# Optimization experiments

Measured on AMD Instinct MI355X. Metric: run time of the kernel, lower is better.

## Reference

```python
import jax, jax.numpy as jnp
import numpy as np

B, T, D = 256, 512, 8      # batch, seq_len, Feature_number
H = 120                    # hidden_size
L = 4                      # layers=['s','s','s','s']
NH = D                     # num_heads = Feature_number
HD = H // NH               # head dim = 15
EPS = 1e-5


def setup_inputs() -> dict:
    key = jax.random.key(0)
    ks = jax.random.split(key, 16)
    rn = lambda k, shape, s=0.1: (jax.random.normal(k, shape, jnp.float32) * s)
    return {
        "x":   jax.random.normal(ks[0], (B, T, D), jnp.float32),
        # input->gate weights, stacked over layers
        "Wi":  rn(ks[1], (L, H, D)),
        "Wf":  rn(ks[2], (L, H, D)),
        "Wz":  rn(ks[3], (L, H, D)),
        "Wo":  rn(ks[4], (L, H, D)),
        # block-diagonal (multi-head) recurrent weights: [L, NH, HD, HD]
        "Ri":  rn(ks[5], (L, NH, HD, HD)),
        "Rf":  rn(ks[6], (L, NH, HD, HD)),
        "Rz":  rn(ks[7], (L, NH, HD, HD)),
        "Ro":  rn(ks[8], (L, NH, HD, HD)),
        "bi":  rn(ks[9],  (L, H), 0.02),
        "bf":  rn(ks[10], (L, H), 0.02),
        "bz":  rn(ks[11], (L, H), 0.02),
        "bo":  rn(ks[12], (L, H), 0.02),
        # per-block down-projection back to Feature_number (residual block)
        "Wp":  rn(ks[13], (L, D, H)),
        "bp":  jnp.zeros((L, D), jnp.float32),
        # BatchNorm1d(Feature_number) affine params
        "gamma": jnp.ones((D,), jnp.float32),
        "beta":  jnp.zeros((D,), jnp.float32),
        # fc5: Linear(Feature_number, 1)
        "Wfc": rn(ks[14], (1, D)),
        "bfc": jnp.zeros((1,), jnp.float32),
    }


def _slstm_layer(x, Wi, Wf, Wz, Wo, Ri, Rf, Rz, Ro, bi, bf, bz, bo, Wp, bp):
    """One sLSTM block: exp-gated recurrence with stabilizer, then down-proj + residual.
    x: [B, T, D] -> [B, T, D]."""
    Bn = x.shape[0]

    def rec(h, R):  # block-diagonal recurrent matmul: [B,H] x [NH,HD,HD] -> [B,H]
        return jnp.einsum("bnd,nde->bne", h.reshape(Bn, NH, HD), R).reshape(Bn, H)

    def step(carry, x_t):
        h, c, n, m = carry                       # each [B, H]
        it = x_t @ Wi.T + rec(h, Ri) + bi        # input gate pre-act
        ft = x_t @ Wf.T + rec(h, Rf) + bf        # forget gate pre-act (exp gating)
        z = jnp.tanh(x_t @ Wz.T + rec(h, Rz) + bz)
        o = jax.nn.sigmoid(x_t @ Wo.T + rec(h, Ro) + bo)
        m_new = jnp.maximum(ft + m, it)          # stabilizer state
        i_p = jnp.exp(it - m_new)
        f_p = jnp.exp(ft + m - m_new)
        c_new = f_p * c + i_p * z
        n_new = f_p * n + i_p                    # normalizer state
        h_new = o * (c_new / n_new)
        return (h_new, c_new, n_new, m_new), h_new

    z0 = jnp.zeros((Bn, H), x.dtype)
    (_, _, _, _), hs = jax.lax.scan(step, (z0, z0, z0, z0), jnp.swapaxes(x, 0, 1))
    y = jnp.einsum("tbh,dh->tbd", hs, Wp) + bp   # down-project to D
    return x + jnp.swapaxes(y, 0, 1)             # residual


def reference(x, Wi, Wf, Wz, Wo, Ri, Rf, Rz, Ro, bi, bf, bz, bo, Wp, bp,
              gamma, beta, Wfc, bfc):
    h = x
    for l in range(L):
        h = _slstm_layer(h, Wi[l], Wf[l], Wz[l], Wo[l], Ri[l], Rf[l], Rz[l], Ro[l],
                         bi[l], bf[l], bz[l], bo[l], Wp[l], bp[l])
    last = h[:, -1, :]                            # [B, D]
    # BatchNorm1d in training mode (batch stats, biased variance)
    mu = jnp.mean(last, axis=0)
    var = jnp.mean((last - mu) ** 2, axis=0)
    bn = (last - mu) / jnp.sqrt(var + EPS) * gamma + beta
    out = jax.nn.sigmoid(bn @ Wfc.T + bfc)        # [B, 1]
    return out[:, 0]                              # squeeze(1) -> [B]
```

## Files before the change

### kernel.cpp

```cpp
#include <hip/hip_runtime.h>
#include <math.h>

#define Bsz 256
#define T   512
#define Dd  8
#define Hh  120
#define Ll  4
#define NHn 8
#define HDd 15
#define HP  20
#define EPSf 1e-5f

__device__ __forceinline__ float fast_rcp(float x) {
#if __has_builtin(__builtin_amdgcn_rcpf)
    return __builtin_amdgcn_rcpf(x);
#else
    return 1.f / x;
#endif
}
__device__ __forceinline__ float tanh_fast(float x) {
    float e = __expf(2.f * x);
    return 1.f - 2.f * fast_rcp(e + 1.f);
}
__device__ __forceinline__ float sigm_fast(float x) {
    return fast_rcp(1.f + __expf(-x));
}

__global__
__attribute__((amdgpu_flat_work_group_size(512, 512)))
__attribute__((amdgpu_waves_per_eu(2, 2)))
void slstm_kernel(
    const float* __restrict__ x,
    const float* __restrict__ Wi, const float* __restrict__ Wf,
    const float* __restrict__ Wz, const float* __restrict__ Wo,
    const float* __restrict__ Ri, const float* __restrict__ Rf,
    const float* __restrict__ Rz, const float* __restrict__ Ro,
    const float* __restrict__ bi, const float* __restrict__ bf,
    const float* __restrict__ bz, const float* __restrict__ bo,
    const float* __restrict__ Wp, const float* __restrict__ bp,
    float* __restrict__ last_out)
{
    __shared__ __align__(16) float xs[T * Dd];
    __shared__ __align__(16) float hb[Ll][2][NHn * HP];

    const int tid = threadIdx.x;
    const int b   = blockIdx.x;
    const int l   = tid >> 7;
    const int j   = tid & 127;

    {
        const float4* xg  = (const float4*)(x + (size_t)b * T * Dd);
        float4*       xs4 = (float4*)xs;
        xs4[tid]       = xg[tid];
        xs4[tid + 512] = xg[tid + 512];
        float* hbf = (float*)hb;
        hbf[tid]       = 0.f;
        hbf[tid + 512] = 0.f;
        if (tid < 256) hbf[tid + 1024] = 0.f;
    }

    const bool gl = (j < Hh);
    const int jj  = gl ? j : 0;
    const int n   = jj / HDd;
    const int e   = jj - n * HDd;
    float wI[Dd], wF[Dd], wZ[Dd], wO[Dd];
    float rI[HDd], rF[HDd], rZ[HDd], rO[HDd];
    {
        const int row = (l * Hh + jj) * Dd;
#pragma unroll
        for (int d = 0; d < Dd; ++d) {
            wI[d] = Wi[row + d]; wF[d] = Wf[row + d];
            wZ[d] = Wz[row + d]; wO[d] = Wo[row + d];
        }
        const int rb = ((l * NHn + n) * HDd) * HDd + e;
#pragma unroll
        for (int d = 0; d < HDd; ++d) {
            rI[d] = Ri[rb + d * HDd]; rF[d] = Rf[rb + d * HDd];
            rZ[d] = Rz[rb + d * HDd]; rO[d] = Ro[rb + d * HDd];
        }
    }
    float bI = bi[l * Hh + jj], bF = bf[l * Hh + jj];
    float bZ = bz[l * Hh + jj], bO = bo[l * Hh + jj];

    const int p  = (j >= 64) ? (j - 64) : j;
    const int d8 = p & 7, ch = p >> 3;
    float wp_r[16];
    {
        const int base = l * Dd * Hh + d8 * Hh + ch * HDd;
#pragma unroll
        for (int k = 0; k < HDd; ++k) wp_r[k] = Wp[base + k];
        wp_r[15] = 0.f;
    }
    float bp_r = bp[l * Dd + d8];

    float cst = 0.f, nst = 0.f, mst = 0.f;

    __syncthreads();

    for (int tau = 0; tau < T + 2 * Ll - 1; ++tau) {
        const int t_g = tau - 2 * l;
        const int t_p = t_g - 1;

        if (gl && (t_g >= 0) && (t_g < T)) {
            const float4* xt4 = (const float4*)(xs + t_g * Dd);
            const float4 xa = xt4[0], xb2 = xt4[1];
            const float xv[Dd] = {xa.x, xa.y, xa.z, xa.w, xb2.x, xb2.y, xb2.z, xb2.w};
            float gi = bI, gf = bF, gz = bZ, go = bO;
#pragma unroll
            for (int d = 0; d < Dd; ++d) {
                gi = fmaf(xv[d], wI[d], gi);
                gf = fmaf(xv[d], wF[d], gf);
                gz = fmaf(xv[d], wZ[d], gz);
                go = fmaf(xv[d], wO[d], go);
            }
            const float4* h4 = (const float4*)(&hb[l][t_g & 1][n * HP]);
            const float4 h0 = h4[0], h1 = h4[1], h2 = h4[2], h3 = h4[3];
            const float hv[16] = {h0.x, h0.y, h0.z, h0.w, h1.x, h1.y, h1.z, h1.w,
                                  h2.x, h2.y, h2.z, h2.w, h3.x, h3.y, h3.z, h3.w};
#pragma unroll
            for (int d = 0; d < HDd; ++d) {
                gi = fmaf(hv[d], rI[d], gi);
                gf = fmaf(hv[d], rF[d], gf);
                gz = fmaf(hv[d], rZ[d], gz);
                go = fmaf(hv[d], rO[d], go);
            }
            const float z  = tanh_fast(gz);
            const float o  = sigm_fast(go);
            const float mn = fmaxf(gf + mst, gi);
            const float ip = __expf(gi - mn);
            const float fp = __expf(gf + mst - mn);
            cst = fmaf(fp, cst, ip * z);
            nst = fmaf(fp, nst, ip);
            mst = mn;
            hb[l][(t_g & 1) ^ 1][n * HP + e] = o * cst * fast_rcp(nst);
        }

        if ((j >= 64) && (t_p >= 0) && (t_p < T)) {
            const float4* h4 = (const float4*)(&hb[l][t_g & 1][ch * HP]);
            const float4 h0 = h4[0], h1 = h4[1], h2 = h4[2], h3 = h4[3];
            const float hv[16] = {h0.x, h0.y, h0.z, h0.w, h1.x, h1.y, h1.z, h1.w,
                                  h2.x, h2.y, h2.z, h2.w, h3.x, h3.y, h3.z, h3.w};
            float s = 0.f;
#pragma unroll
            for (int k = 0; k < 16; ++k) s = fmaf(hv[k], wp_r[k], s);
            s += __shfl_xor(s, 8);
            s += __shfl_xor(s, 16);
            s += __shfl_xor(s, 32);
            if (p < Dd) xs[t_p * Dd + p] += s + bp_r;
        }

        __syncthreads();
    }

    if (tid < Dd) last_out[b * Dd + tid] = xs[(T - 1) * Dd + tid];
}

__global__ __launch_bounds__(Bsz) void bn_fc_kernel(
    const float* __restrict__ last,
    const float* __restrict__ gamma, const float* __restrict__ beta,
    const float* __restrict__ Wfc,   const float* __restrict__ bfc,
    float* __restrict__ out)
{
    __shared__ __align__(16) float ls[Bsz][Dd];
    __shared__ float rsum[32][Dd], rsq[32][Dd];
    __shared__ float mu[Dd], rstdg[Dd], bet[Dd], wfc[Dd];
    const int tid = threadIdx.x;
    {
        const float4* lg = (const float4*)last;
        ((float4*)ls)[tid]       = lg[tid];
        ((float4*)ls)[tid + 256] = lg[tid + 256];
    }
    __syncthreads();
    {
        const int d = tid & 7, g = tid >> 3;
        float s = 0.f, q = 0.f;
#pragma unroll
        for (int k = 0; k < 8; ++k) {
            const float v = ls[g + 32 * k][d];
            s += v; q = fmaf(v, v, q);
        }
        rsum[g][d] = s; rsq[g][d] = q;
    }
    __syncthreads();
    if (tid < Dd) {
        float s = 0.f, q = 0.f;
#pragma unroll
        for (int g = 0; g < 32; ++g) { s += rsum[g][tid]; q += rsq[g][tid]; }
        const float mean = s * (1.f / Bsz);
        const float var  = q * (1.f / Bsz) - mean * mean;
        mu[tid]    = mean;
        rstdg[tid] = rsqrtf(fmaxf(var, 0.f) + EPSf) * gamma[tid];
        bet[tid]   = beta[tid];
        wfc[tid]   = Wfc[tid];
    }
    __syncthreads();
    float acc = bfc[0];
#pragma unroll
    for (int d = 0; d < Dd; ++d)
        acc += ((ls[tid][d] - mu[d]) * rstdg[d] + bet[d]) * wfc[d];
    out[tid] = sigm_fast(acc);
}

extern "C" void kernel_launch(void* const* d_in, const int* in_sizes, int n_in,
                              void* d_out, int out_size, void* d_ws, size_t ws_size,
                              hipStream_t stream) {
    const float* x    = (const float*)d_in[0];
    const float* Wi   = (const float*)d_in[1];
    const float* Wf   = (const float*)d_in[2];
    const float* Wz   = (const float*)d_in[3];
    const float* Wo   = (const float*)d_in[4];
    const float* Ri   = (const float*)d_in[5];
    const float* Rf   = (const float*)d_in[6];
    const float* Rz   = (const float*)d_in[7];
    const float* Ro   = (const float*)d_in[8];
    const float* bi   = (const float*)d_in[9];
    const float* bf   = (const float*)d_in[10];
    const float* bz   = (const float*)d_in[11];
    const float* bo   = (const float*)d_in[12];
    const float* Wp   = (const float*)d_in[13];
    const float* bp   = (const float*)d_in[14];
    const float* gamma= (const float*)d_in[15];
    const float* beta = (const float*)d_in[16];
    const float* Wfc  = (const float*)d_in[17];
    const float* bfc  = (const float*)d_in[18];

    float* last_ws = (float*)d_ws;
    float* out     = (float*)d_out;

    slstm_kernel<<<Bsz, 512, 0, stream>>>(x, Wi, Wf, Wz, Wo, Ri, Rf, Rz, Ro,
                                          bi, bf, bz, bo, Wp, bp, last_ws);
    bn_fc_kernel<<<1, Bsz, 0, stream>>>(last_ws, gamma, beta, Wfc, bfc, out);
}
```

Before: 466.4 us.

## Pack two hidden units per lane and shrink block to one wave per layer

Each layer now runs in a single 64-lane wave, with every active lane computing two hidden units instead of one. The block shrinks from 512 to 256 threads. The down-projection weights move from registers to shared memory so the same wave can also do the projection. This cuts idle lanes and lets the per-layer work stay inside one wavefront, at the cost of twice the serial math per lane per timestep and more register pressure.

Measured after the change: 616.7 us. +32.2%, slower.

```diff
diff --git a/kernel.cpp b/kernel.cpp
--- a/kernel.cpp
+++ b/kernel.cpp
@@ -26,9 +26,48 @@
     return fast_rcp(1.f + __expf(-x));
 }
 
+#define LD16(dst, srcp) { \
+    const float4* _h4 = (const float4*)(srcp); \
+    const float4 _a=_h4[0], _b=_h4[1], _c=_h4[2], _d=_h4[3]; \
+    dst[0]=_a.x; dst[1]=_a.y; dst[2]=_a.z; dst[3]=_a.w; \
+    dst[4]=_b.x; dst[5]=_b.y; dst[6]=_b.z; dst[7]=_b.w; \
+    dst[8]=_c.x; dst[9]=_c.y; dst[10]=_c.z; dst[11]=_c.w; \
+    dst[12]=_d.x; dst[13]=_d.y; dst[14]=_d.z; dst[15]=_d.w; }
+
+__device__ __forceinline__ float unit_step(
+    const float xv[8], const float hv[16],
+    const float w[4][8], const float r[4][15], const float bsc[4],
+    float& c, float& nn, float& m)
+{
+    float gi = bsc[0], gf = bsc[1], gz = bsc[2], go = bsc[3];
+#pragma unroll
+    for (int d = 0; d < 8; ++d) {
+        gi = fmaf(xv[d], w[0][d], gi);
+        gf = fmaf(xv[d], w[1][d], gf);
+        gz = fmaf(xv[d], w[2][d], gz);
+        go = fmaf(xv[d], w[3][d], go);
+    }
+#pragma unroll
+    for (int k = 0; k < 15; ++k) {
+        gi = fmaf(hv[k], r[0][k], gi);
+        gf = fmaf(hv[k], r[1][k], gf);
+        gz = fmaf(hv[k], r[2][k], gz);
+        go = fmaf(hv[k], r[3][k], go);
+    }
+    const float z  = tanh_fast(gz);
+    const float o  = sigm_fast(go);
+    const float mn = fmaxf(gf + m, gi);
+    const float ip = __expf(gi - mn);
+    const float fp = __expf(gf + m - mn);
+    c  = fmaf(fp, c, ip * z);
+    nn = fmaf(fp, nn, ip);
+    m  = mn;
+    return o * c * fast_rcp(nn);
+}
+
 __global__
-__attribute__((amdgpu_flat_work_group_size(512, 512)))
-__attribute__((amdgpu_waves_per_eu(2, 2)))
+__attribute__((amdgpu_flat_work_group_size(256, 256)))
+__attribute__((amdgpu_waves_per_eu(1, 1)))
 void slstm_kernel(
     const float* __restrict__ x,
     const float* __restrict__ Wi, const float* __restrict__ Wf,
@@ -42,58 +81,58 @@
 {
     __shared__ __align__(16) float xs[T * Dd];
     __shared__ __align__(16) float hb[Ll][2][NHn * HP];
-
-    const int tid = threadIdx.x;
-    const int b   = blockIdx.x;
-    const int l   = tid >> 7;
-    const int j   = tid & 127;
+    __shared__ __align__(16) float wp_s[Ll][Dd][NHn][16];
+
+    const int tid  = threadIdx.x;
+    const int b    = blockIdx.x;
+    const int l    = tid >> 6;
+    const int lane = tid & 63;
 
     {
-        const float4* xg  = (const float4*)(x + (size_t)b * T * Dd);
-        float4*       xs4 = (float4*)xs;
-        xs4[tid]       = xg[tid];
-        xs4[tid + 512] = xg[tid + 512];
+        const float4* xg = (const float4*)(x + (size_t)b * T * Dd);
+        float4* xs4 = (float4*)xs;
+#pragma unroll
+        for (int i = 0; i < 4; ++i) xs4[tid + 256 * i] = xg[tid + 256 * i];
         float* hbf = (float*)hb;
-        hbf[tid]       = 0.f;
-        hbf[tid + 512] = 0.f;
-        if (tid < 256) hbf[tid + 1024] = 0.f;
-    }
-
-    const bool gl = (j < Hh);
-    const int jj  = gl ? j : 0;
-    const int n   = jj / HDd;
-    const int e   = jj - n * HDd;
-    float wI[Dd], wF[Dd], wZ[Dd], wO[Dd];
-    float rI[HDd], rF[HDd], rZ[HDd], rO[HDd];
-    {
-        const int row = (l * Hh + jj) * Dd;
-#pragma unroll
-        for (int d = 0; d < Dd; ++d) {
-            wI[d] = Wi[row + d]; wF[d] = Wf[row + d];
-            wZ[d] = Wz[row + d]; wO[d] = Wo[row + d];
-        }
-        const int rb = ((l * NHn + n) * HDd) * HDd + e;
-#pragma unroll
-        for (int d = 0; d < HDd; ++d) {
-            rI[d] = Ri[rb + d * HDd]; rF[d] = Rf[rb + d * HDd];
-            rZ[d] = Rz[rb + d * HDd]; rO[d] = Ro[rb + d * HDd];
-        }
-    }
-    float bI = bi[l * Hh + jj], bF = bf[l * Hh + jj];
-    float bZ = bz[l * Hh + jj], bO = bo[l * Hh + jj];
-
-    const int p  = (j >= 64) ? (j - 64) : j;
-    const int d8 = p & 7, ch = p >> 3;
-    float wp_r[16];
-    {
-        const int base = l * Dd * Hh + d8 * Hh + ch * HDd;
-#pragma unroll
-        for (int k = 0; k < HDd; ++k) wp_r[k] = Wp[base + k];
-        wp_r[15] = 0.f;
-    }
-    float bp_r = bp[l * Dd + d8];
-
-    float cst = 0.f, nst = 0.f, mst = 0.f;
+#pragma unroll
+        for (int i = 0; i < 5; ++i) hbf[tid + 256 * i] = 0.f;
+        for (int i = tid; i < Ll * Dd * NHn * 16; i += 256) {
+            const int k  = i & 15;
+            const int ch = (i >> 4) & 7;
+            const int d  = (i >> 7) & 7;
+            const int ll = i >> 10;
+            ((float*)wp_s)[i] = (k < 15) ? Wp[ll * Dd * Hh + d * Hh + ch * HDd + k] : 0.f;
+        }
+    }
+
+    const bool act = (lane < 60);
+    const int u0 = act ? 2 * lane     : 0;
+    const int u1 = act ? 2 * lane + 1 : 1;
+    const int n0 = u0 / HDd, e0 = u0 - HDd * n0;
+    const int n1 = u1 / HDd, e1 = u1 - HDd * n1;
+
+    const float* Wg[4] = {Wi, Wf, Wz, Wo};
+    const float* Rg[4] = {Ri, Rf, Rz, Ro};
+    const float* bg[4] = {bi, bf, bz, bo};
+
+    float ww0[4][8], ww1[4][8], rr0[4][15], rr1[4][15], bb0[4], bb1[4];
+#pragma unroll
+    for (int g = 0; g < 4; ++g) {
+        const int row0 = (l * Hh + u0) * Dd, row1 = (l * Hh + u1) * Dd;
+#pragma unroll
+        for (int d = 0; d < 8; ++d) { ww0[g][d] = Wg[g][row0 + d]; ww1[g][d] = Wg[g][row1 + d]; }
+        const int rb0 = ((l * NHn + n0) * HDd) * HDd + e0;
+        const int rb1 = ((l * NHn + n1) * HDd) * HDd + e1;
+#pragma unroll
+        for (int k = 0; k < 15; ++k) { rr0[g][k] = Rg[g][rb0 + k * HDd]; rr1[g][k] = Rg[g][rb1 + k * HDd]; }
+        bb0[g] = bg[g][l * Hh + u0]; bb1[g] = bg[g][l * Hh + u1];
+    }
+
+    const int ch = lane >> 3, d8 = lane & 7;
+    const float bp_r = bp[l * Dd + d8];
+
+    float c0 = 0.f, ns0 = 0.f, m0 = 0.f;
+    float c1 = 0.f, ns1 = 0.f, m1 = 0.f;
 
     __syncthreads();
 
@@ -101,52 +140,36 @@
         const int t_g = tau - 2 * l;
         const int t_p = t_g - 1;
 
-        if (gl && (t_g >= 0) && (t_g < T)) {
-            const float4* xt4 = (const float4*)(xs + t_g * Dd);
-            const float4 xa = xt4[0], xb2 = xt4[1];
-            const float xv[Dd] = {xa.x, xa.y, xa.z, xa.w, xb2.x, xb2.y, xb2.z, xb2.w};
-            float gi = bI, gf = bF, gz = bZ, go = bO;
-#pragma unroll
-            for (int d = 0; d < Dd; ++d) {
-                gi = fmaf(xv[d], wI[d], gi);
-                gf = fmaf(xv[d], wF[d], gf);
-                gz = fmaf(xv[d], wZ[d], gz);
-                go = fmaf(xv[d], wO[d], go);
+        if (act && (t_g >= 0) && (t_g < T)) {
+            float xv[8];
+            {
+                const float4* xt4 = (const float4*)(xs + t_g * Dd);
+                const float4 xa = xt4[0], xb2 = xt4[1];
+                xv[0]=xa.x; xv[1]=xa.y; xv[2]=xa.z; xv[3]=xa.w;
+                xv[4]=xb2.x; xv[5]=xb2.y; xv[6]=xb2.z; xv[7]=xb2.w;
             }
-            const float4* h4 = (const float4*)(&hb[l][t_g & 1][n * HP]);
-            const float4 h0 = h4[0], h1 = h4[1], h2 = h4[2], h3 = h4[3];
-            const float hv[16] = {h0.x, h0.y, h0.z, h0.w, h1.x, h1.y, h1.z, h1.w,
-                                  h2.x, h2.y, h2.z, h2.w, h3.x, h3.y, h3.z, h3.w};
-#pragma unroll
-            for (int d = 0; d < HDd; ++d) {
-                gi = fmaf(hv[d], rI[d], gi);
-                gf = fmaf(hv[d], rF[d], gf);
-                gz = fmaf(hv[d], rZ[d], gz);
-                go = fmaf(hv[d], rO[d], go);
-            }
-            const float z  = tanh_fast(gz);
-            const float o  = sigm_fast(go);
-            const float mn = fmaxf(gf + mst, gi);
-            const float ip = __expf(gi - mn);
-            const float fp = __expf(gf + mst - mn);
-            cst = fmaf(fp, cst, ip * z);
-            nst = fmaf(fp, nst, ip);
-            mst = mn;
-            hb[l][(t_g & 1) ^ 1][n * HP + e] = o * cst * fast_rcp(nst);
-        }
-
-        if ((j >= 64) && (t_p >= 0) && (t_p < T)) {
-            const float4* h4 = (const float4*)(&hb[l][t_g & 1][ch * HP]);
-            const float4 h0 = h4[0], h1 = h4[1], h2 = h4[2], h3 = h4[3];
-            const float hv[16] = {h0.x, h0.y, h0.z, h0.w, h1.x, h1.y, h1.z, h1.w,
-                                  h2.x, h2.y, h2.z, h2.w, h3.x, h3.y, h3.z, h3.w};
+            const float* hbase = hb[l][t_g & 1];
+            float hv0[16], hv1[16];
+            LD16(hv0, hbase + n0 * HP);
+            LD16(hv1, hbase + n1 * HP);
+            const float h0n = unit_step(xv, hv0, ww0, rr0, bb0, c0, ns0, m0);
+            const float h1n = unit_step(xv, hv1, ww1, rr1, bb1, c1, ns1, m1);
+            float* hw = hb[l][(t_g & 1) ^ 1];
+            hw[n0 * HP + e0] = h0n;
+            hw[n1 * HP + e1] = h1n;
+        }
+
+        if ((t_p >= 0) && (t_p < T)) {
+            float hr[16], wr[16];
+            LD16(hr, hb[l][t_g & 1] + ch * HP);
+            LD16(wr, &wp_s[l][d8][ch][0]);
             float s = 0.f;
 #pragma unroll
-            for (int k = 0; k < 16; ++k) s = fmaf(hv[k], wp_r[k], s);
+            for (int k = 0; k < 15; ++k) s = fmaf(hr[k], wr[k], s);
             s += __shfl_xor(s, 8);
             s += __shfl_xor(s, 16);
             s += __shfl_xor(s, 32);
-            if (p < Dd) xs[t_p * Dd + p] += s + bp_r;
+            if (lane < Dd) xs[t_p * Dd + lane] += s + bp_r;
         }
 
         __syncthreads();
@@ -227,7 +250,7 @@
     float* last_ws = (float*)d_ws;
     float* out     = (float*)d_out;
 
-    slstm_kernel<<<Bsz, 512, 0, stream>>>(x, Wi, Wf, Wz, Wo, Ri, Rf, Rz, Ro,
+    slstm_kernel<<<Bsz, 256, 0, stream>>>(x, Wi, Wf, Wz, Wo, Ri, Rf, Rz, Ro,
                                           bi, bf, bz, bo, Wp, bp, last_ws);
     bn_fc_kernel<<<1, Bsz, 0, stream>>>(last_ws, gamma, beta, Wfc, bfc, out);
 }
```
